# Kernel optimization log

Hardware: AMD Instinct MI355X
Metric: run time of the kernel (lower is better)

## Reference

```python
import jax, jax.numpy as jnp
import numpy as np

DIM = 512
NUM_HEADS = 8
HEAD_DIM = DIM // NUM_HEADS
SCALE = HEAD_DIM ** (-0.5)
EPS = 1e-12  # torch F.normalize eps


def setup_inputs() -> dict:
    key = jax.random.key(0)
    ks = jax.random.split(key, 6)
    B, C, H, W = 8, DIM, 64, 64
    x = jax.random.normal(ks[0], (B, C, H, W), dtype=jnp.float32)
    mask = jax.random.uniform(ks[1], (B, 1, H, W), dtype=jnp.float32)
    s = DIM ** -0.5
    Wq = jax.random.normal(ks[2], (DIM, DIM), dtype=jnp.float32) * s
    Wk = jax.random.normal(ks[3], (DIM, DIM), dtype=jnp.float32) * s
    Wv = jax.random.normal(ks[4], (DIM, DIM), dtype=jnp.float32) * s
    Wp = jax.random.normal(ks[5], (DIM, DIM), dtype=jnp.float32) * s
    return {"x": x, "mask": mask, "Wq": Wq, "Wk": Wk, "Wv": Wv, "Wp": Wp}


def _split_heads(t, B, HW):
    # [B, HW, C] -> [B, heads, head_dim, HW]
    return t.reshape(B, HW, NUM_HEADS, HEAD_DIM).transpose(0, 2, 3, 1)


def _l2norm(t):
    # torch F.normalize: x / max(||x||, eps) along last axis
    n = jnp.sqrt(jnp.sum(t * t, axis=-1, keepdims=True))
    return t / jnp.maximum(n, EPS)


def reference(x, mask, Wq, Wk, Wv, Wp):
    B, C, H, W = x.shape
    HW = H * W
    xm = x * mask                             # masked input for q, k
    # NCHW -> [B, HW, C]
    xt = x.transpose(0, 2, 3, 1).reshape(B, HW, C)
    xmt = xm.transpose(0, 2, 3, 1).reshape(B, HW, C)
    q = _split_heads(xmt @ Wq.T, B, HW)       # [B, h, d, HW]
    k = _split_heads(xmt @ Wk.T, B, HW)
    v = _split_heads(xt @ Wv.T, B, HW)
    q = _l2norm(q)
    k = _l2norm(k)
    # channel-wise attention: [B, h, d, d]
    attn = jnp.einsum('bhcn,bhdn->bhcd', q, k) * SCALE
    attn = jax.nn.softmax(attn, axis=-1)
    out = jnp.einsum('bhcd,bhdn->bhcn', attn, v)  # [B, h, d, HW]
    out = out.transpose(0, 3, 1, 2).reshape(B, HW, C)  # [B, HW, C]
    out = out @ Wp.T
    return out.reshape(B, H, W, C).transpose(0, 3, 1, 2)  # NCHW
```

## Files before the change

kernel.cpp:

```cpp
#include <hip/hip_runtime.h>
#include <math.h>

#define DIMC 512
#define HW 4096
#define SCALE 0.125f
#define EPSN 1e-12f

typedef __attribute__((ext_vector_type(8))) short bf16x8;
typedef __attribute__((ext_vector_type(4))) float f32x4;

__device__ __forceinline__ unsigned short f2bf(float f) {
    union { float f; unsigned int u; } v; v.f = f;
    unsigned int u = v.u;
    return (unsigned short)((u + 0x7fffu + ((u >> 16) & 1u)) >> 16);
}
__device__ __forceinline__ float bf2f(unsigned short h) {
    union { unsigned int u; float f; } v; v.u = ((unsigned int)h) << 16;
    return v.f;
}

union Pack8 { int4 v; unsigned short u[8]; };

__device__ __forceinline__ void gload_lds16(const unsigned short* src, char* ldst) {
    __builtin_amdgcn_global_load_lds(
        (const __attribute__((address_space(1))) void*)src,
        (__attribute__((address_space(3))) void*)ldst, 16, 0, 0);
}

__global__ __launch_bounds__(256) void prep_wx(
    const float* __restrict__ Wq, const float* __restrict__ Wk,
    const float* __restrict__ Wv, const float* __restrict__ Wp,
    const float* __restrict__ x, const float* __restrict__ mask,
    unsigned short* __restrict__ Wb, unsigned short* __restrict__ WvT,
    unsigned short* __restrict__ Wpb,
    unsigned short* __restrict__ xT, unsigned short* __restrict__ xmb)
{
    const int blk = blockIdx.x;
    const int t = threadIdx.x;
    if (blk < 512) {
        int i = (blk * 256 + t) * 4;
        const float* s = (i < 262144) ? Wq : Wk;
        int off = i & 262143;
        float4 v4 = *(const float4*)(s + off);
        ushort4 o;
        o.x = f2bf(v4.x); o.y = f2bf(v4.y); o.z = f2bf(v4.z); o.w = f2bf(v4.w);
        *(ushort4*)(Wb + i) = o;
    } else if (blk < 576) {
        const int bb = blk - 512;
        const int cp0 = (bb >> 3) * 64;
        const int c30 = (bb & 7) * 64;
        __shared__ unsigned short sT[64][65];
        #pragma unroll
        for (int i = 0; i < 4; ++i) {
            int ch = t + i * 256;
            int r = ch >> 4, col4 = (ch & 15) * 4;
            float4 v4 = *(const float4*)(Wv + (size_t)(cp0 + r) * DIMC + c30 + col4);
            sT[r][col4 + 0] = f2bf(v4.x); sT[r][col4 + 1] = f2bf(v4.y);
            sT[r][col4 + 2] = f2bf(v4.z); sT[r][col4 + 3] = f2bf(v4.w);
        }
        __syncthreads();
        #pragma unroll
        for (int i = 0; i < 2; ++i) {
            int ch = t + i * 256;
            int n = ch >> 3, cc = (ch & 7) * 8;
            Pack8 pk;
            #pragma unroll
            for (int e = 0; e < 8; ++e) pk.u[e] = sT[cc + e][n];
            *(int4*)(WvT + (size_t)(c30 + n) * DIMC + cp0 + cc) = pk.v;
        }
    } else if (blk < 832) {
        int i = ((blk - 576) * 256 + t) * 4;
        float4 v4 = *(const float4*)(Wp + i);
        ushort4 o;
        o.x = f2bf(v4.x); o.y = f2bf(v4.y); o.z = f2bf(v4.z); o.w = f2bf(v4.w);
        *(ushort4*)(Wpb + i) = o;
    } else {
        const int idx = blk - 832;
        const int n0 = (idx & 63) * 64;
        const int c0 = ((idx >> 6) & 7) * 64;
        const int b  = idx >> 9;
        __shared__ unsigned short sT[64][65];
        #pragma unroll
        for (int i = 0; i < 4; ++i) {
            int ch = t + i * 256;
            int r = ch >> 4, col4 = (ch & 15) * 4;
            float4 v4 = *(const float4*)(x + ((size_t)b * DIMC + c0 + r) * HW + n0 + col4);
            sT[r][col4 + 0] = f2bf(v4.x); sT[r][col4 + 1] = f2bf(v4.y);
            sT[r][col4 + 2] = f2bf(v4.z); sT[r][col4 + 3] = f2bf(v4.w);
            float4 mv = *(const float4*)(mask + (size_t)b * HW + n0 + col4);
            ushort4 xm;
            xm.x = f2bf(v4.x * mv.x); xm.y = f2bf(v4.y * mv.y);
            xm.z = f2bf(v4.z * mv.z); xm.w = f2bf(v4.w * mv.w);
            *(ushort4*)(xmb + ((size_t)b * DIMC + c0 + r) * HW + n0 + col4) = xm;
        }
        __syncthreads();
        #pragma unroll
        for (int i = 0; i < 2; ++i) {
            int ch = t + i * 256;
            int n = ch >> 3, cc = (ch & 7) * 8;
            Pack8 pk;
            #pragma unroll
            for (int e = 0; e < 8; ++e) pk.u[e] = sT[cc + e][n];
            *(int4*)(xT + ((size_t)b * HW + n0 + n) * DIMC + c0 + cc) = pk.v;
        }
    }
}

__global__ __launch_bounds__(256) void gram_mfma(
    const unsigned short* __restrict__ xmb, unsigned short* __restrict__ Gpart)
{
    const int f = blockIdx.x;
    const int r8 = f & 7, q = f >> 3;
    const int pair = q >> 2;
    const int grp  = r8 + ((q & 3) << 3);
    const int b  = grp & 7;
    const int sp = grp >> 3;
    const int TA[10] = {0,0,0,0,1,1,1,2,2,3};
    const int TB[10] = {0,1,2,3,1,2,3,2,3,3};
    const int cA0 = TA[pair] * 128;
    const int cB0 = TB[pair] * 128;
    const unsigned short* A = xmb + (size_t)b * DIMC * HW + (size_t)cA0 * HW + sp * 1024;
    const unsigned short* B = xmb + (size_t)b * DIMC * HW + (size_t)cB0 * HW + sp * 1024;

    __shared__ __align__(16) char sm[65536];

    const int t = threadIdx.x, lane = t & 63, w = t >> 6;
    const int wm = w >> 1, wn = w & 1;
    const int rsub = lane >> 3;
    const int srccol = ((lane & 7) ^ rsub) << 3;

    f32x4 zero = {0.f, 0.f, 0.f, 0.f};
    f32x4 acc[4][4];
    #pragma unroll
    for (int m = 0; m < 4; ++m)
        #pragma unroll
        for (int n = 0; n < 4; ++n) acc[m][n] = zero;

    #define STAGE_G(buf, c0)                                                  \
        {                                                                     \
            char* dst = sm + (buf) * 32768;                                   \
            _Pragma("unroll")                                                 \
            for (int i = 0; i < 4; ++i) {                                     \
                int ii = w * 4 + i;                                           \
                gload_lds16(A + (size_t)(ii * 8 + rsub) * HW + (c0) + srccol, \
                            dst + ii * 1024);                                 \
                gload_lds16(B + (size_t)(ii * 8 + rsub) * HW + (c0) + srccol, \
                            dst + 16384 + ii * 1024);                         \
            }                                                                 \
        }

    STAGE_G(0, 0);
    int cur = 0;
    for (int c0 = 0; c0 < 1024; c0 += 64) {
        __syncthreads();
        if (c0 + 64 < 1024) STAGE_G(cur ^ 1, c0 + 64);
        const char* sA = sm + cur * 32768;
        const char* sB = sA + 16384;
        #pragma unroll
        for (int s = 0; s < 2; ++s) {
            bf16x8 af[4], bfr[4];
            #pragma unroll
            for (int m = 0; m < 4; ++m) {
                int r = wm * 64 + m * 16 + (lane & 15);
                int byte = r * 128 + s * 64 + ((lane >> 4) << 4);
                byte ^= (r & 7) << 4;
                af[m] = *(const bf16x8*)(sA + byte);
            }
            #pragma unroll
            for (int n = 0; n < 4; ++n) {
                int r = wn * 64 + n * 16 + (lane & 15);
                int byte = r * 128 + s * 64 + ((lane >> 4) << 4);
                byte ^= (r & 7) << 4;
                bfr[n] = *(const bf16x8*)(sB + byte);
            }
            #pragma unroll
            for (int m = 0; m < 4; ++m)
                #pragma unroll
                for (int n = 0; n < 4; ++n)
                    acc[m][n] = __builtin_amdgcn_mfma_f32_16x16x32_bf16(
                        af[m], bfr[n], acc[m][n], 0, 0, 0);
        }
        cur ^= 1;
    }
    #undef STAGE_G

    unsigned short* st = (unsigned short*)sm;
    __syncthreads();
    #pragma unroll
    for (int m = 0; m < 4; ++m)
        #pragma unroll
        for (int n = 0; n < 4; ++n)
            #pragma unroll
            for (int r4 = 0; r4 < 4; ++r4) {
                int jl = wm * 64 + m * 16 + ((lane >> 4) << 2) + r4;
                int nl = wn * 64 + n * 16 + (lane & 15);
                st[jl * 136 + nl] = f2bf(acc[m][n][r4]);
            }
    __syncthreads();
    unsigned short* Gp = Gpart + ((size_t)(sp * 8 + b) * 10 + pair) * 16384;
    #pragma unroll
    for (int it = 0; it < 8; ++it) {
        int idx = t + it * 256, jl = idx >> 4, l16 = idx & 15;
        int4 pv = *(int4*)((char*)sm + jl * 272 + l16 * 16);
        *(int4*)(Gp + (size_t)jl * 128 + l16 * 8) = pv;
    }
}

__global__ __launch_bounds__(256) void gram_reduce_sym(
    const unsigned short* __restrict__ Gpart, unsigned short* __restrict__ G)
{
    const int pair = blockIdx.x;
    const int b    = blockIdx.y;
    const int TA[10] = {0,0,0,0,1,1,1,2,2,3};
    const int TB[10] = {0,1,2,3,1,2,3,2,3,3};
    const int ta = TA[pair], tb = TB[pair];
    const int t = threadIdx.x;

    __shared__ unsigned short sT[128][130];
    unsigned short* Gb = G + (size_t)b * DIMC * DIMC;

    #pragma unroll
    for (int ch = 0; ch < 8; ++ch) {
        int e = ch * 2048 + t * 8;
        int i = e >> 7, j = e & 127;
        Pack8 p0, p1, p2, p3, o;
        p0.v = *(const int4*)(Gpart + ((size_t)(0 * 8 + b) * 10 + pair) * 16384 + e);
        p1.v = *(const int4*)(Gpart + ((size_t)(1 * 8 + b) * 10 + pair) * 16384 + e);
        p2.v = *(const int4*)(Gpart + ((size_t)(2 * 8 + b) * 10 + pair) * 16384 + e);
        p3.v = *(const int4*)(Gpart + ((size_t)(3 * 8 + b) * 10 + pair) * 16384 + e);
        #pragma unroll
        for (int k = 0; k < 8; ++k) {
            unsigned short s = f2bf(bf2f(p0.u[k]) + bf2f(p1.u[k]) + bf2f(p2.u[k]) + bf2f(p3.u[k]));
            o.u[k] = s;
            sT[i][j + k] = s;
        }
        *(int4*)(Gb + (size_t)(ta * 128 + i) * DIMC + tb * 128 + j) = o.v;
    }
    if (ta != tb) {
        __syncthreads();
        #pragma unroll
        for (int ch = 0; ch < 8; ++ch) {
            int e = ch * 2048 + t * 8;
            int i2 = e >> 7, j2 = e & 127;
            Pack8 o;
            #pragma unroll
            for (int k = 0; k < 8; ++k) o.u[k] = sT[j2 + k][i2];
            *(int4*)(Gb + (size_t)(tb * 128 + i2) * DIMC + ta * 128 + j2) = o.v;
        }
    }
}

__global__ __launch_bounds__(256) void gemm_nn_128(
    const unsigned short* __restrict__ Ag, size_t aBatch,
    const unsigned short* __restrict__ Bg, size_t bBatch,
    unsigned short* __restrict__ Cg, size_t cBatch)
{
    const int b  = blockIdx.z;
    const int j0 = blockIdx.y * 128;
    const int n0 = blockIdx.x * 128;
    const unsigned short* A = Ag + (size_t)b * aBatch + (size_t)j0 * DIMC;
    const unsigned short* B = Bg + (size_t)b * bBatch + (size_t)n0 * DIMC;

    __shared__ __align__(16) char sm[65536];

    const int t = threadIdx.x, lane = t & 63, w = t >> 6;
    const int wm = w >> 1, wn = w & 1;
    const int rsub = lane >> 3;
    const int srccol = ((lane & 7) ^ rsub) << 3;

    f32x4 zero = {0.f, 0.f, 0.f, 0.f};
    f32x4 acc[4][4];
    #pragma unroll
    for (int m = 0; m < 4; ++m)
        #pragma unroll
        for (int n = 0; n < 4; ++n) acc[m][n] = zero;

    #define STAGE_NN(buf, c0)                                                   \
        {                                                                       \
            char* dst = sm + (buf) * 32768;                                     \
            _Pragma("unroll")                                                   \
            for (int i = 0; i < 4; ++i) {                                       \
                int ii = w * 4 + i;                                             \
                gload_lds16(A + (size_t)(ii * 8 + rsub) * DIMC + (c0) + srccol, \
                            dst + ii * 1024);                                   \
                gload_lds16(B + (size_t)(ii * 8 + rsub) * DIMC + (c0) + srccol, \
                            dst + 16384 + ii * 1024);                           \
            }                                                                   \
        }

    STAGE_NN(0, 0);
    int cur = 0;
    for (int c0 = 0; c0 < DIMC; c0 += 64) {
        __syncthreads();
        if (c0 + 64 < DIMC) STAGE_NN(cur ^ 1, c0 + 64);
        const char* sA = sm + cur * 32768;
        const char* sB = sA + 16384;
        #pragma unroll
        for (int s = 0; s < 2; ++s) {
            bf16x8 af[4], bfr[4];
            #pragma unroll
            for (int m = 0; m < 4; ++m) {
                int r = wm * 64 + m * 16 + (lane & 15);
                int byte = r * 128 + s * 64 + ((lane >> 4) << 4);
                byte ^= (r & 7) << 4;
                af[m] = *(const bf16x8*)(sA + byte);
            }
            #pragma unroll
            for (int n = 0; n < 4; ++n) {
                int r = wn * 64 + n * 16 + (lane & 15);
                int byte = r * 128 + s * 64 + ((lane >> 4) << 4);
                byte ^= (r & 7) << 4;
                bfr[n] = *(const bf16x8*)(sB + byte);
            }
            #pragma unroll
            for (int m = 0; m < 4; ++m)
                #pragma unroll
                for (int n = 0; n < 4; ++n)
                    acc[m][n] = __builtin_amdgcn_mfma_f32_16x16x32_bf16(
                        af[m], bfr[n], acc[m][n], 0, 0, 0);
        }
        cur ^= 1;
    }
    #undef STAGE_NN

    unsigned short* st = (unsigned short*)sm;
    __syncthreads();
    #pragma unroll
    for (int m = 0; m < 4; ++m)
        #pragma unroll
        for (int n = 0; n < 4; ++n)
            #pragma unroll
            for (int r4 = 0; r4 < 4; ++r4) {
                int jl = wm * 64 + m * 16 + ((lane >> 4) << 2) + r4;
                int nl = wn * 64 + n * 16 + (lane & 15);
                st[jl * 136 + nl] = f2bf(acc[m][n][r4]);
            }
    __syncthreads();
    #pragma unroll
    for (int it = 0; it < 8; ++it) {
        int idx = t + it * 256, jl = idx >> 4, l16 = idx & 15;
        int4 pv = *(int4*)((char*)sm + jl * 272 + l16 * 16);
        *(int4*)(Cg + (size_t)b * cBatch + (size_t)(j0 + jl) * DIMC + n0 + l16 * 8) = pv;
    }
}

__global__ __launch_bounds__(256) void s_softmax(
    const unsigned short* __restrict__ TU, const unsigned short* __restrict__ Wb,
    unsigned short* __restrict__ attnT)
{
    const int bh = blockIdx.x;
    const int b = bh >> 3, h = bh & 7;
    const unsigned short* A = TU + ((size_t)b * 1024 + h * 64) * DIMC;
    const unsigned short* B = Wb + 262144 + (size_t)(h * 64) * DIMC;

    __shared__ __align__(16) char sm[32768];
    __shared__ float sS[64][65];
    __shared__ float srq[64];
    __shared__ float srk[64];
    __shared__ unsigned short aT[64][65];

    const int t = threadIdx.x, lane = t & 63, w = t >> 6;
    const int wm = w >> 1, wn = w & 1;
    const int rsub = lane >> 3;
    const int srccol = ((lane & 7) ^ rsub) << 3;

    {
        const int rid  = t >> 1;
        const int half = t & 1;
        const int isK  = (rid >= 64);
        const int rl   = rid & 63;
        const unsigned short* ar = TU + ((size_t)b * 1024 + (isK ? 512 : 0) + h * 64 + rl) * DIMC
                                 + half * 256;
        const unsigned short* wr = Wb + (isK ? 262144 : 0) + (size_t)(h * 64 + rl) * DIMC
                                 + half * 256;
        float s = 0.f;
        #pragma unroll 8
        for (int i = 0; i < 32; ++i) {
            Pack8 pa, pw;
            pa.v = *(const int4*)(ar + i * 8);
            pw.v = *(const int4*)(wr + i * 8);
            #pragma unroll
            for (int e = 0; e < 8; ++e) s = fmaf(bf2f(pa.u[e]), bf2f(pw.u[e]), s);
        }
        s += __shfl_xor(s, 1, 2);
        if (half == 0) {
            float r = 1.0f / fmaxf(sqrtf(s), EPSN);
            if (isK) srk[rl] = r; else srq[rl] = r;
        }
    }

    f32x4 zero = {0.f, 0.f, 0.f, 0.f};
    f32x4 acc[2][2];
    #pragma unroll
    for (int m = 0; m < 2; ++m)
        #pragma unroll
        for (int n = 0; n < 2; ++n) acc[m][n] = zero;

    #define STAGE_S(buf, c0)                                                    \
        {                                                                       \
            char* dst = sm + (buf) * 16384;                                     \
            _Pragma("unroll")                                                   \
            for (int i = 0; i < 2; ++i) {                                       \
                int ii = w * 2 + i;                                             \
                gload_lds16(A + (size_t)(ii * 8 + rsub) * DIMC + (c0) + srccol, \
                            dst + ii * 1024);                                   \
                gload_lds16(B + (size_t)(ii * 8 + rsub) * DIMC + (c0) + srccol, \
                            dst + 8192 + ii * 1024);                            \
            }                                                                   \
        }

    STAGE_S(0, 0);
    int cur = 0;
    for (int c0 = 0; c0 < DIMC; c0 += 64) {
        __syncthreads();
        if (c0 + 64 < DIMC) STAGE_S(cur ^ 1, c0 + 64);
        const char* sA = sm + cur * 16384;
        const char* sB = sA + 8192;
        #pragma unroll
        for (int s = 0; s < 2; ++s) {
            bf16x8 aq[2], bk[2];
            #pragma unroll
            for (int m = 0; m < 2; ++m) {
                int r = wm * 32 + m * 16 + (lane & 15);
                int byte = r * 128 + s * 64 + ((lane >> 4) << 4);
                byte ^= (r & 7) << 4;
                aq[m] = *(const bf16x8*)(sA + byte);
            }
            #pragma unroll
            for (int n = 0; n < 2; ++n) {
                int r = wn * 32 + n * 16 + (lane & 15);
                int byte = r * 128 + s * 64 + ((lane >> 4) << 4);
                byte ^= (r & 7) << 4;
                bk[n] = *(const bf16x8*)(sB + byte);
            }
            #pragma unroll
            for (int m = 0; m < 2; ++m)
                #pragma unroll
                for (int n = 0; n < 2; ++n)
                    acc[m][n] = __builtin_amdgcn_mfma_f32_16x16x32_bf16(
                        aq[m], bk[n], acc[m][n], 0, 0, 0);
        }
        cur ^= 1;
    }
    #undef STAGE_S

    #pragma unroll
    for (int m = 0; m < 2; ++m)
        #pragma unroll
        for (int n = 0; n < 2; ++n)
            #pragma unroll
            for (int r4 = 0; r4 < 4; ++r4) {
                int r = wm * 32 + m * 16 + ((lane >> 4) << 2) + r4;
                int c = wn * 32 + n * 16 + (lane & 15);
                sS[r][c] = acc[m][n][r4];
            }
    __syncthreads();

    const int r = t >> 2;
    const int p = t & 3;
    const float rq = srq[r];
    float row[16];
    #pragma unroll
    for (int c = 0; c < 16; ++c)
        row[c] = sS[r][p * 16 + c] * SCALE * rq * srk[p * 16 + c];
    float mx = row[0];
    #pragma unroll
    for (int c = 1; c < 16; ++c) mx = fmaxf(mx, row[c]);
    mx = fmaxf(mx, __shfl_xor(mx, 1, 4));
    mx = fmaxf(mx, __shfl_xor(mx, 2, 4));
    float sum = 0.f;
    #pragma unroll
    for (int c = 0; c < 16; ++c) { row[c] = __expf(row[c] - mx); sum += row[c]; }
    sum += __shfl_xor(sum, 1, 4);
    sum += __shfl_xor(sum, 2, 4);
    const float inv = 1.0f / sum;
    #pragma unroll
    for (int i = 0; i < 16; ++i)
        aT[p * 16 + i][r] = f2bf(row[i] * inv);
    __syncthreads();
    {
        const int d  = t >> 2;
        const int ch = t & 3;
        Pack8 o0, o1;
        #pragma unroll
        for (int e = 0; e < 8; ++e) { o0.u[e] = aT[d][ch * 16 + e]; o1.u[e] = aT[d][ch * 16 + 8 + e]; }
        unsigned short* dst = attnT + (((size_t)bh * 64) + d) * 64 + ch * 16;
        *(int4*)(dst)     = o0.v;
        *(int4*)(dst + 8) = o1.v;
    }
}

__global__ __launch_bounds__(256) void wp2_mfma(
    const unsigned short* __restrict__ Wpb, const unsigned short* __restrict__ attnT,
    unsigned short* __restrict__ Wp2b)
{
    const int j0 = blockIdx.x * 128;
    const int h  = blockIdx.y;
    const int b  = blockIdx.z;
    const unsigned short* A = Wpb + (size_t)j0 * DIMC + h * 64;
    const unsigned short* B = attnT + (size_t)(b * 8 + h) * 4096;

    __shared__ __align__(16) char sm[24576];

    const int t = threadIdx.x, lane = t & 63, w = t >> 6;
    const int rsub = lane >> 3;
    const int srccol = ((lane & 7) ^ rsub) << 3;

    #pragma unroll
    for (int i = 0; i < 4; ++i) {
        int ii = w * 4 + i;
        gload_lds16(A + (size_t)(ii * 8 + rsub) * DIMC + srccol, sm + ii * 1024);
    }
    #pragma unroll
    for (int i = 0; i < 2; ++i) {
        int ii = w * 2 + i;
        gload_lds16(B + (size_t)(ii * 8 + rsub) * 64 + srccol, sm + 16384 + ii * 1024);
    }
    __syncthreads();

    f32x4 zero = {0.f, 0.f, 0.f, 0.f};
    f32x4 acc[2][4];
    #pragma unroll
    for (int m = 0; m < 2; ++m)
        #pragma unroll
        for (int n = 0; n < 4; ++n) acc[m][n] = zero;

    #pragma unroll
    for (int s = 0; s < 2; ++s) {
        bf16x8 af[2], bfr[4];
        #pragma unroll
        for (int m = 0; m < 2; ++m) {
            int r = w * 32 + m * 16 + (lane & 15);
            int byte = r * 128 + s * 64 + ((lane >> 4) << 4);
            byte ^= (r & 7) << 4;
            af[m] = *(const bf16x8*)(sm + byte);
        }
        #pragma unroll
        for (int n = 0; n < 4; ++n) {
            int r = n * 16 + (lane & 15);
            int byte = r * 128 + s * 64 + ((lane >> 4) << 4);
            byte ^= (r & 7) << 4;
            bfr[n] = *(const bf16x8*)(sm + 16384 + byte);
        }
        #pragma unroll
        for (int m = 0; m < 2; ++m)
            #pragma unroll
            for (int n = 0; n < 4; ++n)
                acc[m][n] = __builtin_amdgcn_mfma_f32_16x16x32_bf16(
                    af[m], bfr[n], acc[m][n], 0, 0, 0);
    }

    unsigned short* st = (unsigned short*)sm;
    __syncthreads();
    #pragma unroll
    for (int m = 0; m < 2; ++m)
        #pragma unroll
        for (int n = 0; n < 4; ++n)
            #pragma unroll
            for (int r4 = 0; r4 < 4; ++r4) {
                int jl = w * 32 + m * 16 + ((lane >> 4) << 2) + r4;
                int dl = n * 16 + (lane & 15);
                st[jl * 72 + dl] = f2bf(acc[m][n][r4]);
            }
    __syncthreads();
    #pragma unroll
    for (int it = 0; it < 4; ++it) {
        int idx = t + it * 256, jl = idx >> 3, ch = idx & 7;
        int4 pv = *(int4*)((char*)sm + jl * 144 + ch * 16);
        *(int4*)(Wp2b + ((size_t)b * DIMC + j0 + jl) * DIMC + h * 64 + ch * 8) = pv;
    }
}

__global__ __launch_bounds__(256) void final_mfma(
    const unsigned short* __restrict__ Wfb, const unsigned short* __restrict__ xT,
    float* __restrict__ out)
{
    const int f = blockIdx.x;
    const int r8 = f & 7, q = f >> 3;
    const int jt = q & 3;
    const int nt = r8 + (((q >> 2) & 3) << 3);
    const int b  = q >> 4;
    const int j0 = jt * 128;
    const int n0 = nt * 128;
    const unsigned short* A = Wfb + (size_t)b * DIMC * DIMC + (size_t)j0 * DIMC;
    const unsigned short* B = xT + (size_t)b * HW * DIMC + (size_t)n0 * DIMC;

    __shared__ __align__(16) char sm[65536];

    const int t = threadIdx.x, lane = t & 63, w = t >> 6;
    const int wm = w >> 1, wn = w & 1;
    const int rsub = lane >> 3;
    const int srccol = ((lane & 7) ^ rsub) << 3;

    f32x4 zero = {0.f, 0.f, 0.f, 0.f};
    f32x4 acc[4][4];
    #pragma unroll
    for (int m = 0; m < 4; ++m)
        #pragma unroll
        for (int n = 0; n < 4; ++n) acc[m][n] = zero;

    #define STAGE_FIN(buf, c0)                                                  \
        {                                                                       \
            char* dst = sm + (buf) * 32768;                                     \
            _Pragma("unroll")                                                   \
            for (int i = 0; i < 4; ++i) {                                       \
                int ii = w * 4 + i;                                             \
                gload_lds16(A + (size_t)(ii * 8 + rsub) * DIMC + (c0) + srccol, \
                            dst + ii * 1024);                                   \
                gload_lds16(B + (size_t)(ii * 8 + rsub) * DIMC + (c0) + srccol, \
                            dst + 16384 + ii * 1024);                           \
            }                                                                   \
        }

    STAGE_FIN(0, 0);
    int cur = 0;
    for (int c0 = 0; c0 < DIMC; c0 += 64) {
        __syncthreads();
        if (c0 + 64 < DIMC) STAGE_FIN(cur ^ 1, c0 + 64);
        const char* sA = sm + cur * 32768;
        const char* sB = sA + 16384;
        #pragma unroll
        for (int s = 0; s < 2; ++s) {
            bf16x8 af[4], bfr[4];
            #pragma unroll
            for (int m = 0; m < 4; ++m) {
                int r = wm * 64 + m * 16 + (lane & 15);
                int byte = r * 128 + s * 64 + ((lane >> 4) << 4);
                byte ^= (r & 7) << 4;
                af[m] = *(const bf16x8*)(sA + byte);
            }
            #pragma unroll
            for (int n = 0; n < 4; ++n) {
                int r = wn * 64 + n * 16 + (lane & 15);
                int byte = r * 128 + s * 64 + ((lane >> 4) << 4);
                byte ^= (r & 7) << 4;
                bfr[n] = *(const bf16x8*)(sB + byte);
            }
            #pragma unroll
            for (int m = 0; m < 4; ++m)
                #pragma unroll
                for (int n = 0; n < 4; ++n)
                    acc[m][n] = __builtin_amdgcn_mfma_f32_16x16x32_bf16(
                        af[m], bfr[n], acc[m][n], 0, 0, 0);
        }
        cur ^= 1;
    }
    #undef STAGE_FIN

    #pragma unroll
    for (int m = 0; m < 4; ++m)
        #pragma unroll
        for (int r4 = 0; r4 < 4; ++r4) {
            int j = j0 + wm * 64 + m * 16 + ((lane >> 4) << 2) + r4;
            size_t rowbase = ((size_t)b * DIMC + j) * HW + n0 + wn * 64 + (lane & 15);
            #pragma unroll
            for (int n = 0; n < 4; ++n)
                out[rowbase + n * 16] = acc[m][n][r4];
        }
}

extern "C" void kernel_launch(void* const* d_in, const int* in_sizes, int n_in,
                              void* d_out, int out_size, void* d_ws, size_t ws_size,
                              hipStream_t stream)
{
    const float* x    = (const float*)d_in[0];
    const float* mask = (const float*)d_in[1];
    const float* Wq   = (const float*)d_in[2];
    const float* Wk   = (const float*)d_in[3];
    const float* Wv   = (const float*)d_in[4];
    const float* Wp   = (const float*)d_in[5];
    float* out = (float*)d_out;
    char* wsb = (char*)d_ws;

    unsigned short* xT   = (unsigned short*)(wsb + 0);
    unsigned short* xmb  = (unsigned short*)(wsb + 67108864);
    unsigned short* Wb   = (unsigned short*)(wsb + 134217728);
    unsigned short* WvT  = (unsigned short*)(wsb + 135266304);
    unsigned short* Wpb  = (unsigned short*)(wsb + 135790592);
    unsigned short* G    = (unsigned short*)(wsb + 136314880);
    unsigned short* TU   = (unsigned short*)(wsb + 140509184);
    unsigned short* attnT= (unsigned short*)(wsb + 148897792);
    unsigned short* Wp2b = (unsigned short*)(wsb + 149422080);
    unsigned short* Wfb  = (unsigned short*)(wsb + 153616384);
    unsigned short* Gpart= (unsigned short*)(wsb + 157810688);

    prep_wx        <<<4928,            256, 0, stream>>>(Wq, Wk, Wv, Wp, x, mask,
                                                         Wb, WvT, Wpb, xT, xmb);
    gram_mfma      <<<320,             256, 0, stream>>>(xmb, Gpart);
    gram_reduce_sym<<<dim3(10, 8),     256, 0, stream>>>(Gpart, G);
    gemm_nn_128    <<<dim3(4, 8, 8),   256, 0, stream>>>(Wb, (size_t)0, G, (size_t)(DIMC*DIMC), TU, (size_t)(1024*DIMC));
    s_softmax      <<<64,              256, 0, stream>>>(TU, Wb, attnT);
    wp2_mfma       <<<dim3(4, 8, 8),   256, 0, stream>>>(Wpb, attnT, Wp2b);
    gemm_nn_128    <<<dim3(4, 4, 8),   256, 0, stream>>>(Wp2b, (size_t)(DIMC*DIMC), WvT, (size_t)0, Wfb, (size_t)(DIMC*DIMC));
    final_mfma     <<<1024,            256, 0, stream>>>(Wfb, xT, out);
}
```

Measured before the change: 112.1 us.

## Fuse softmax with Wp·attn product and flatten gemm grid with batch-interleaved order

The softmax kernel now writes the attention matrix into a swizzled shared-memory buffer. It then computes the Wp×attn product in place, looping over four 128-row tiles, which removes the wp2_mfma launch and the attnT global round trip. The gemm_nn_128 grid is flattened to 1D with batch as the fastest index, which changes block scheduling and cache locality. The trade-off is that the fused stage runs on only 64 blocks doing serial work, where the old kernel spread it over 256 blocks.

```diff
diff --git a/kernel.cpp b/kernel.cpp
--- a/kernel.cpp
+++ b/kernel.cpp
@@ -253,11 +253,13 @@
 __global__ __launch_bounds__(256) void gemm_nn_128(
     const unsigned short* __restrict__ Ag, size_t aBatch,
     const unsigned short* __restrict__ Bg, size_t bBatch,
-    unsigned short* __restrict__ Cg, size_t cBatch)
+    unsigned short* __restrict__ Cg, size_t cBatch, int nn)
 {
-    const int b  = blockIdx.z;
-    const int j0 = blockIdx.y * 128;
-    const int n0 = blockIdx.x * 128;
+    const int f = blockIdx.x;
+    const int b = f & 7;
+    const int inner = f >> 3;
+    const int j0 = (inner / nn) * 128;
+    const int n0 = (inner % nn) * 128;
     const unsigned short* A = Ag + (size_t)b * aBatch + (size_t)j0 * DIMC;
     const unsigned short* B = Bg + (size_t)b * bBatch + (size_t)n0 * DIMC;
 
@@ -344,9 +346,9 @@
     }
 }
 
-__global__ __launch_bounds__(256) void s_softmax(
+__global__ __launch_bounds__(256) void s_softmax_wp2(
     const unsigned short* __restrict__ TU, const unsigned short* __restrict__ Wb,
-    unsigned short* __restrict__ attnT)
+    const unsigned short* __restrict__ Wpb, unsigned short* __restrict__ Wp2b)
 {
     const int bh = blockIdx.x;
     const int b = bh >> 3, h = bh & 7;
@@ -357,7 +359,7 @@
     __shared__ float sS[64][65];
     __shared__ float srq[64];
     __shared__ float srk[64];
-    __shared__ unsigned short aT[64][65];
+    __shared__ __align__(16) unsigned short aSwz[4096];
 
     const int t = threadIdx.x, lane = t & 63, w = t >> 6;
     const int wm = w >> 1, wn = w & 1;
@@ -456,118 +458,94 @@
             }
     __syncthreads();
 
-    const int r = t >> 2;
-    const int p = t & 3;
-    const float rq = srq[r];
-    float row[16];
-    #pragma unroll
-    for (int c = 0; c < 16; ++c)
-        row[c] = sS[r][p * 16 + c] * SCALE * rq * srk[p * 16 + c];
-    float mx = row[0];
-    #pragma unroll
-    for (int c = 1; c < 16; ++c) mx = fmaxf(mx, row[c]);
-    mx = fmaxf(mx, __shfl_xor(mx, 1, 4));
-    mx = fmaxf(mx, __shfl_xor(mx, 2, 4));
-    float sum = 0.f;
-    #pragma unroll
-    for (int c = 0; c < 16; ++c) { row[c] = __expf(row[c] - mx); sum += row[c]; }
-    sum += __shfl_xor(sum, 1, 4);
-    sum += __shfl_xor(sum, 2, 4);
-    const float inv = 1.0f / sum;
-    #pragma unroll
-    for (int i = 0; i < 16; ++i)
-        aT[p * 16 + i][r] = f2bf(row[i] * inv);
+    {
+        const int r = t >> 2;
+        const int p = t & 3;
+        const float rq = srq[r];
+        float row[16];
+        #pragma unroll
+        for (int c = 0; c < 16; ++c)
+            row[c] = sS[r][p * 16 + c] * SCALE * rq * srk[p * 16 + c];
+        float mx = row[0];
+        #pragma unroll
+        for (int c = 1; c < 16; ++c) mx = fmaxf(mx, row[c]);
+        mx = fmaxf(mx, __shfl_xor(mx, 1, 4));
+        mx = fmaxf(mx, __shfl_xor(mx, 2, 4));
+        float sum = 0.f;
+        #pragma unroll
+        for (int c = 0; c < 16; ++c) { row[c] = __expf(row[c] - mx); sum += row[c]; }
+        sum += __shfl_xor(sum, 1, 4);
+        sum += __shfl_xor(sum, 2, 4);
+        const float inv = 1.0f / sum;
+        #pragma unroll
+        for (int i = 0; i < 16; ++i) {
+            int d = p * 16 + i;
+            int ei = (((r >> 3) ^ (d & 7)) << 3) + (r & 7);
+            aSwz[d * 64 + ei] = f2bf(row[i] * inv);
+        }
+    }
     __syncthreads();
-    {
-        const int d  = t >> 2;
-        const int ch = t & 3;
-        Pack8 o0, o1;
-        #pragma unroll
-        for (int e = 0; e < 8; ++e) { o0.u[e] = aT[d][ch * 16 + e]; o1.u[e] = aT[d][ch * 16 + 8 + e]; }
-        unsigned short* dst = attnT + (((size_t)bh * 64) + d) * 64 + ch * 16;
-        *(int4*)(dst)     = o0.v;
-        *(int4*)(dst + 8) = o1.v;
-    }
-}
-
-__global__ __launch_bounds__(256) void wp2_mfma(
-    const unsigned short* __restrict__ Wpb, const unsigned short* __restrict__ attnT,
-    unsigned short* __restrict__ Wp2b)
-{
-    const int j0 = blockIdx.x * 128;
-    const int h  = blockIdx.y;
-    const int b  = blockIdx.z;
-    const unsigned short* A = Wpb + (size_t)j0 * DIMC + h * 64;
-    const unsigned short* B = attnT + (size_t)(b * 8 + h) * 4096;
-
-    __shared__ __align__(16) char sm[24576];
-
-    const int t = threadIdx.x, lane = t & 63, w = t >> 6;
-    const int rsub = lane >> 3;
-    const int srccol = ((lane & 7) ^ rsub) << 3;
-
-    #pragma unroll
-    for (int i = 0; i < 4; ++i) {
-        int ii = w * 4 + i;
-        gload_lds16(A + (size_t)(ii * 8 + rsub) * DIMC + srccol, sm + ii * 1024);
-    }
-    #pragma unroll
-    for (int i = 0; i < 2; ++i) {
-        int ii = w * 2 + i;
-        gload_lds16(B + (size_t)(ii * 8 + rsub) * 64 + srccol, sm + 16384 + ii * 1024);
-    }
-    __syncthreads();
-
-    f32x4 zero = {0.f, 0.f, 0.f, 0.f};
-    f32x4 acc[2][4];
-    #pragma unroll
-    for (int m = 0; m < 2; ++m)
-        #pragma unroll
-        for (int n = 0; n < 4; ++n) acc[m][n] = zero;
-
-    #pragma unroll
-    for (int s = 0; s < 2; ++s) {
-        bf16x8 af[2], bfr[4];
-        #pragma unroll
-        for (int m = 0; m < 2; ++m) {
-            int r = w * 32 + m * 16 + (lane & 15);
-            int byte = r * 128 + s * 64 + ((lane >> 4) << 4);
-            byte ^= (r & 7) << 4;
-            af[m] = *(const bf16x8*)(sm + byte);
-        }
-        #pragma unroll
-        for (int n = 0; n < 4; ++n) {
-            int r = n * 16 + (lane & 15);
-            int byte = r * 128 + s * 64 + ((lane >> 4) << 4);
-            byte ^= (r & 7) << 4;
-            bfr[n] = *(const bf16x8*)(sm + 16384 + byte);
-        }
+
+    for (int jt = 0; jt < 4; ++jt) {
+        const unsigned short* Ap = Wpb + (size_t)(jt * 128) * DIMC + h * 64;
+        #pragma unroll
+        for (int i = 0; i < 4; ++i) {
+            int ii = w * 4 + i;
+            gload_lds16(Ap + (size_t)(ii * 8 + rsub) * DIMC + srccol, sm + ii * 1024);
+        }
+        __syncthreads();
+
+        f32x4 acc2[2][4];
         #pragma unroll
         for (int m = 0; m < 2; ++m)
             #pragma unroll
+            for (int n = 0; n < 4; ++n) acc2[m][n] = zero;
+
+        #pragma unroll
+        for (int s = 0; s < 2; ++s) {
+            bf16x8 af[2], bfr[4];
+            #pragma unroll
+            for (int m = 0; m < 2; ++m) {
+                int r = w * 32 + m * 16 + (lane & 15);
+                int byte = r * 128 + s * 64 + ((lane >> 4) << 4);
+                byte ^= (r & 7) << 4;
+                af[m] = *(const bf16x8*)(sm + byte);
+            }
+            #pragma unroll
+            for (int n = 0; n < 4; ++n) {
+                int r = n * 16 + (lane & 15);
+                int byte = r * 128 + s * 64 + ((lane >> 4) << 4);
+                byte ^= (r & 7) << 4;
+                bfr[n] = *(const bf16x8*)((const char*)aSwz + byte);
+            }
+            #pragma unroll
+            for (int m = 0; m < 2; ++m)
+                #pragma unroll
+                for (int n = 0; n < 4; ++n)
+                    acc2[m][n] = __builtin_amdgcn_mfma_f32_16x16x32_bf16(
+                        af[m], bfr[n], acc2[m][n], 0, 0, 0);
+        }
+        __syncthreads();
+
+        unsigned short* st = (unsigned short*)sm;
+        #pragma unroll
+        for (int m = 0; m < 2; ++m)
+            #pragma unroll
             for (int n = 0; n < 4; ++n)
-                acc[m][n] = __builtin_amdgcn_mfma_f32_16x16x32_bf16(
-                    af[m], bfr[n], acc[m][n], 0, 0, 0);
-    }
-
-    unsigned short* st = (unsigned short*)sm;
-    __syncthreads();
-    #pragma unroll
-    for (int m = 0; m < 2; ++m)
-        #pragma unroll
-        for (int n = 0; n < 4; ++n)
-            #pragma unroll
-            for (int r4 = 0; r4 < 4; ++r4) {
-                int jl = w * 32 + m * 16 + ((lane >> 4) << 2) + r4;
-                int dl = n * 16 + (lane & 15);
-                st[jl * 72 + dl] = f2bf(acc[m][n][r4]);
-            }
-    __syncthreads();
-    #pragma unroll
-    for (int it = 0; it < 4; ++it) {
-        int idx = t + it * 256, jl = idx >> 3, ch = idx & 7;
-        int4 pv = *(int4*)((char*)sm + jl * 144 + ch * 16);
-        *(int4*)(Wp2b + ((size_t)b * DIMC + j0 + jl) * DIMC + h * 64 + ch * 8) = pv;
+                #pragma unroll
+                for (int r4 = 0; r4 < 4; ++r4) {
+                    int jl = w * 32 + m * 16 + ((lane >> 4) << 2) + r4;
+                    int dl = n * 16 + (lane & 15);
+                    st[jl * 72 + dl] = f2bf(acc2[m][n][r4]);
+                }
+        __syncthreads();
+        #pragma unroll
+        for (int it = 0; it < 4; ++it) {
+            int idx = t + it * 256, jl = idx >> 3, ch = idx & 7;
+            int4 pv = *(int4*)((char*)sm + jl * 144 + ch * 16);
+            *(int4*)(Wp2b + ((size_t)b * DIMC + jt * 128 + jl) * DIMC + h * 64 + ch * 8) = pv;
+        }
+        __syncthreads();
     }
 }
 
@@ -679,7 +657,6 @@
     unsigned short* Wpb  = (unsigned short*)(wsb + 135790592);
     unsigned short* G    = (unsigned short*)(wsb + 136314880);
     unsigned short* TU   = (unsigned short*)(wsb + 140509184);
-    unsigned short* attnT= (unsigned short*)(wsb + 148897792);
     unsigned short* Wp2b = (unsigned short*)(wsb + 149422080);
     unsigned short* Wfb  = (unsigned short*)(wsb + 153616384);
     unsigned short* Gpart= (unsigned short*)(wsb + 157810688);
@@ -688,9 +665,8 @@
                                                          Wb, WvT, Wpb, xT, xmb);
     gram_mfma      <<<320,             256, 0, stream>>>(xmb, Gpart);
     gram_reduce_sym<<<dim3(10, 8),     256, 0, stream>>>(Gpart, G);
-    gemm_nn_128    <<<dim3(4, 8, 8),   256, 0, stream>>>(Wb, (size_t)0, G, (size_t)(DIMC*DIMC), TU, (size_t)(1024*DIMC));
-    s_softmax      <<<64,              256, 0, stream>>>(TU, Wb, attnT);
-    wp2_mfma       <<<dim3(4, 8, 8),   256, 0, stream>>>(Wpb, attnT, Wp2b);
-    gemm_nn_128    <<<dim3(4, 4, 8),   256, 0, stream>>>(Wp2b, (size_t)(DIMC*DIMC), WvT, (size_t)0, Wfb, (size_t)(DIMC*DIMC));
+    gemm_nn_128    <<<256,             256, 0, stream>>>(Wb, (size_t)0, G, (size_t)(DIMC*DIMC), TU, (size_t)(1024*DIMC), 4);
+    s_softmax_wp2  <<<64,              256, 0, stream>>>(TU, Wb, Wpb, Wp2b);
+    gemm_nn_128    <<<128,             256, 0, stream>>>(Wp2b, (size_t)(DIMC*DIMC), WvT, (size_t)0, Wfb, (size_t)(DIMC*DIMC), 4);
     final_mfma     <<<1024,            256, 0, stream>>>(Wfb, xT, out);
 }
```

Result: no change. 113.7 us (+1.5%).
